# Performance work log

Measured on AMD Instinct MI355X. Metric: run time of the kernel, lower is better.

The kernel has to match this reference:

```python
import jax, jax.numpy as jnp
import numpy as np

HIDDEN = 768
HEADS = 12
HEAD_DIM = HIDDEN // HEADS


def setup_inputs() -> dict:
    key = jax.random.key(0)
    ks = jax.random.split(key, 6)
    B, N = 32, 577  # N = 1 CLS + 576 patches
    x = jax.random.normal(ks[0], (B, N, HIDDEN), dtype=jnp.float32)
    seg_bias = jax.random.uniform(ks[1], (B, N - 1), dtype=jnp.float32)
    w_qkv = jax.random.normal(ks[2], (HIDDEN, 3 * HIDDEN), dtype=jnp.float32) * 0.02
    b_qkv = jnp.zeros((3 * HIDDEN,), dtype=jnp.float32)
    w_proj = jax.random.normal(ks[3], (HIDDEN, HIDDEN), dtype=jnp.float32) * 0.02
    b_proj = jnp.zeros((HIDDEN,), dtype=jnp.float32)
    seg_scale = jnp.ones((), dtype=jnp.float32)
    return {"x": x, "seg_bias": seg_bias, "w_qkv": w_qkv, "b_qkv": b_qkv,
            "w_proj": w_proj, "b_proj": b_proj, "seg_scale": seg_scale}


def reference(x, seg_bias, w_qkv, b_qkv, w_proj, b_proj, seg_scale):
    B, N, _ = x.shape
    scale = HEAD_DIM ** -0.5
    qkv = x @ w_qkv + b_qkv                       # (B, N, 3*H*D)
    qkv = qkv.reshape(B, N, 3, HEADS, HEAD_DIM)
    q = qkv[:, :, 0].transpose(0, 2, 1, 3)        # (B, H, N, D)
    k = qkv[:, :, 1].transpose(0, 2, 1, 3)
    v = qkv[:, :, 2].transpose(0, 2, 1, 3)
    attn = jnp.einsum('bhqd,bhkd->bhqk', q, k) * scale  # (B, H, N, N)
    # additive seg bias on CLS-query row, patch keys only (cols 1:)
    bias = (seg_bias * seg_scale)[:, None, None, :]     # (B,1,1,N-1)
    attn = attn.at[:, :, 0:1, 1:].add(bias)
    attn = jax.nn.softmax(attn, axis=-1)
    out = jnp.einsum('bhqk,bhkd->bhqd', attn, v)        # (B, H, N, D)
    out = out.transpose(0, 2, 1, 3).reshape(B, N, HIDDEN)
    return out @ w_proj + b_proj
```

## Files before the change

### kernel.cpp

```cpp
#include <hip/hip_runtime.h>


typedef unsigned short bf16_t;
typedef __attribute__((ext_vector_type(8))) short short8;
typedef __attribute__((ext_vector_type(4))) float f32x4;

#define B_    32
#define N_    577
#define BN_   18464
#define HID_  768
#define NH_   12
#define HD_   64
#define QKVC_ 2304
#define NPAD_ 640

__device__ __forceinline__ bf16_t f2bf(float f) {
  union { float f; unsigned u; } x; x.f = f;
  unsigned r = x.u + 0x7fffu + ((x.u >> 16) & 1u);
  return (bf16_t)(r >> 16);
}

__global__ __launch_bounds__(256) void cast_kernel(const float* __restrict__ in,
                                                   bf16_t* __restrict__ out, int n4) {
  int i = blockIdx.x * 256 + threadIdx.x;
  if (i >= n4) return;
  float4 v = ((const float4*)in)[i];
  ushort4 o;
  o.x = f2bf(v.x); o.y = f2bf(v.y); o.z = f2bf(v.z); o.w = f2bf(v.w);
  ((ushort4*)out)[i] = o;
}

__global__ __launch_bounds__(256) void transpose_cast_kernel(const float* __restrict__ in,
                                                             bf16_t* __restrict__ out,
                                                             int R, int C) {
  __shared__ float tile[32][33];
  int c0 = blockIdx.x * 32, r0 = blockIdx.y * 32;
  int tx = threadIdx.x, ty = threadIdx.y;
  #pragma unroll
  for (int i = ty; i < 32; i += 8)
    tile[i][tx] = in[(size_t)(r0 + i) * C + c0 + tx];
  __syncthreads();
  #pragma unroll
  for (int i = ty; i < 32; i += 8)
    out[(size_t)(c0 + i) * R + r0 + tx] = f2bf(tile[tx][i]);
}

template <int OUT_BF16>
__global__ __launch_bounds__(256, 3) void gemm_bf16_kernel(
    const bf16_t* __restrict__ A,
    const bf16_t* __restrict__ Bt,
    const float* __restrict__ bias,
    void* __restrict__ Cout,
    int M, int Nc) {
  __shared__ bf16_t As[128 * 64];
  __shared__ bf16_t Bs[128 * 64];

  const int tid  = threadIdx.x;
  const int lane = tid & 63, w = tid >> 6;
  const int quad = lane >> 4, l16 = lane & 15;

  const int Mb = (M + 127) >> 7;
  const int Nb = Nc >> 7;
  const int np_full = Mb >> 3;
  const int rem = Mb - np_full * 8;
  int bid = blockIdx.x;
  int m_blk, n_blk;
  int body = np_full * 8 * Nb;
  if (bid < body) {
    int p = bid / (8 * Nb), local = bid % (8 * Nb);
    m_blk = p * 8 + (local & 7);
    n_blk = local >> 3;
  } else {
    int t = bid - body;
    m_blk = np_full * 8 + t % rem;
    n_blk = t / rem;
  }
  const int m0 = m_blk * 128, n0 = n_blk * 128;
  const int wm = (w >> 1) * 64, wn = (w & 1) * 64;

  f32x4 acc[4][4];
  #pragma unroll
  for (int i = 0; i < 4; ++i)
    #pragma unroll
    for (int j = 0; j < 4; ++j)
      acc[i][j] = (f32x4){0.f, 0.f, 0.f, 0.f};

  for (int kt = 0; kt < 768; kt += 64) {
    __syncthreads();
    #pragma unroll
    for (int it = 0; it < 4; ++it) {
      int gi = it * 256 + tid;
      int row = gi >> 3, chp = gi & 7;
      int ch = chp ^ (row & 7);
      int gm = m0 + row; if (gm >= M) gm = M - 1;
      __builtin_amdgcn_global_load_lds(
          (const __attribute__((address_space(1))) unsigned int*)(A + (size_t)gm * 768 + kt + ch * 8),
          (__attribute__((address_space(3))) unsigned int*)(As + gi * 8),
          16, 0, 0);
      int gn = n0 + row;
      __builtin_amdgcn_global_load_lds(
          (const __attribute__((address_space(1))) unsigned int*)(Bt + (size_t)gn * 768 + kt + ch * 8),
          (__attribute__((address_space(3))) unsigned int*)(Bs + gi * 8),
          16, 0, 0);
    }
    __syncthreads();

    #pragma unroll
    for (int ks = 0; ks < 2; ++ks) {
      short8 af[4], bfr[4];
      #pragma unroll
      for (int i = 0; i < 4; ++i) {
        int row = wm + i * 16 + l16;
        int c = ks * 4 + quad;
        af[i] = *(const short8*)(As + row * 64 + (c ^ (row & 7)) * 8);
      }
      #pragma unroll
      for (int j = 0; j < 4; ++j) {
        int row = wn + j * 16 + l16;
        int c = ks * 4 + quad;
        bfr[j] = *(const short8*)(Bs + row * 64 + (c ^ (row & 7)) * 8);
      }
      #pragma unroll
      for (int i = 0; i < 4; ++i)
        #pragma unroll
        for (int j = 0; j < 4; ++j)
          acc[i][j] = __builtin_amdgcn_mfma_f32_16x16x32_bf16(af[i], bfr[j], acc[i][j], 0, 0, 0);
    }
  }

  #pragma unroll
  for (int i = 0; i < 4; ++i) {
    int mrow_base = m0 + wm + i * 16 + quad * 4;
    #pragma unroll
    for (int j = 0; j < 4; ++j) {
      int col = n0 + wn + j * 16 + l16;
      float bs = bias[col];
      #pragma unroll
      for (int r = 0; r < 4; ++r) {
        int row = mrow_base + r;
        if (row < M) {
          float v = acc[i][j][r] + bs;
          if (OUT_BF16)
            ((bf16_t*)Cout)[(size_t)row * Nc + col] = f2bf(v);
          else
            ((float*)Cout)[(size_t)row * Nc + col] = v;
        }
      }
    }
  }
}

__global__ __launch_bounds__(256) void vt_kernel(const bf16_t* __restrict__ qkv,
                                                 bf16_t* __restrict__ vT) {
  const int t = blockIdx.x, h = blockIdx.y, b = blockIdx.z;
  const int tid = threadIdx.x;
  __shared__ bf16_t Ls[64 * 65];
  const int kv0 = t * 64;
  const bf16_t* Vp = qkv + (size_t)b * N_ * QKVC_ + 2 * HID_ + h * HD_;

  #pragma unroll
  for (int it = 0; it < 2; ++it) {
    int idx = it * 256 + tid;
    int row = idx >> 3, ch = idx & 7;
    int krow = kv0 + row; if (krow > N_ - 1) krow = N_ - 1;
    short8 v8 = *(const short8*)(Vp + (size_t)krow * QKVC_ + ch * 8);
    #pragma unroll
    for (int j = 0; j < 8; ++j)
      Ls[(ch * 8 + j) * 65 + row] = (bf16_t)v8[j];
  }
  __syncthreads();
  bf16_t* outp = vT + ((size_t)(b * NH_ + h) * HD_) * NPAD_;
  #pragma unroll
  for (int it = 0; it < 2; ++it) {
    int idx = it * 256 + tid;
    int d = idx >> 3, kc = idx & 7;
    short8 o8;
    #pragma unroll
    for (int j = 0; j < 8; ++j)
      o8[j] = (short)Ls[d * 65 + kc * 8 + j];
    *(short8*)(outp + (size_t)d * NPAD_ + kv0 + kc * 8) = o8;
  }
}

__global__ __launch_bounds__(256) void attn_kernel(
    const bf16_t* __restrict__ qkv,
    const bf16_t* __restrict__ vT,
    const float* __restrict__ seg_bias,
    const float* __restrict__ seg_scale,
    bf16_t* __restrict__ out) {
  const int bid  = blockIdx.x;
  const int pair = bid % (B_ * NH_);
  const int qt   = bid / (B_ * NH_);
  const int h    = pair % NH_;
  const int b    = pair / NH_;
  const int tid = threadIdx.x;
  const int w = tid >> 6, lane = tid & 63;
  const int quad = lane >> 4, l16 = lane & 15;

  __shared__ bf16_t Ks[2][64 * 72];
  __shared__ bf16_t Vt[2][64 * 72];
  __shared__ bf16_t Pb[4][32 * 72];

  const bf16_t* Qbase = qkv + (size_t)b * N_ * QKVC_ + h * HD_;
  const bf16_t* Kbase = Qbase + HID_;
  const bf16_t* Vtb   = vT + ((size_t)(b * NH_ + h) * HD_) * NPAD_;

  const int q0 = qt * 128 + w * 32;
  short8 qf[2][2];
  #pragma unroll
  for (int mi = 0; mi < 2; ++mi) {
    int qr = q0 + mi * 16 + l16;
    if (qr > N_ - 1) qr = N_ - 1;
    qf[mi][0] = *(const short8*)(Qbase + (size_t)qr * QKVC_ + quad * 8);
    qf[mi][1] = *(const short8*)(Qbase + (size_t)qr * QKVC_ + 32 + quad * 8);
  }
  const float qsc = 0.125f * 1.44269504f;
  #pragma unroll
  for (int mi = 0; mi < 2; ++mi)
    #pragma unroll
    for (int c = 0; c < 2; ++c)
      #pragma unroll
      for (int j = 0; j < 8; ++j) {
        unsigned u = ((unsigned)(unsigned short)qf[mi][c][j]) << 16;
        union { unsigned u; float f; } x; x.u = u;
        qf[mi][c][j] = (short)f2bf(x.f * qsc);
      }

  f32x4 o[2][4];
  float lsum[2][4];
  #pragma unroll
  for (int mi = 0; mi < 2; ++mi)
    #pragma unroll
    for (int j = 0; j < 4; ++j) {
      o[mi][j] = (f32x4){0.f, 0.f, 0.f, 0.f};
      lsum[mi][j] = 0.f;
    }

  const float ssl = seg_scale[0] * 1.44269504f;
  const bool bias_wave = (qt == 0 && w == 0);
  bf16_t* pw = Pb[w];

  const int srow = tid >> 3;
  const int sch  = tid & 7;

  short8 kpre[2], vpre[2];
  #pragma unroll
  for (int it = 0; it < 2; ++it) {
    int row = it * 32 + srow;
    int krow = row; if (krow > N_ - 1) krow = N_ - 1;
    kpre[it] = *(const short8*)(Kbase + (size_t)krow * QKVC_ + sch * 8);
    vpre[it] = *(const short8*)(Vtb + (size_t)row * NPAD_ + sch * 8);
  }
  #pragma unroll
  for (int it = 0; it < 2; ++it) {
    int row = it * 32 + srow;
    *(short8*)(&Ks[0][0] + row * 72 + sch * 8) = kpre[it];
    *(short8*)(&Vt[0][0] + row * 72 + sch * 8) = vpre[it];
  }
  __syncthreads();

  for (int t = 0; t < 10; ++t) {
    const int cur = t & 1;
    const int kv0 = t * 64;
    const bf16_t* ks = &Ks[cur][0];
    const bf16_t* vt = &Vt[cur][0];

    if (t < 9) {
      const int kv1 = kv0 + 64;
      #pragma unroll
      for (int it = 0; it < 2; ++it) {
        int row = it * 32 + srow;
        int krow = kv1 + row; if (krow > N_ - 1) krow = N_ - 1;
        kpre[it] = *(const short8*)(Kbase + (size_t)krow * QKVC_ + sch * 8);
        vpre[it] = *(const short8*)(Vtb + (size_t)row * NPAD_ + kv1 + sch * 8);
      }
    }

    f32x4 s[2][4];
    #pragma unroll
    for (int mi = 0; mi < 2; ++mi)
      #pragma unroll
      for (int sub = 0; sub < 4; ++sub)
        s[mi][sub] = (f32x4){0.f, 0.f, 0.f, 0.f};
    #pragma unroll
    for (int sub = 0; sub < 4; ++sub) {
      short8 k0 = *(const short8*)(ks + (sub * 16 + l16) * 72 + quad * 8);
      short8 k1 = *(const short8*)(ks + (sub * 16 + l16) * 72 + 32 + quad * 8);
      #pragma unroll
      for (int mi = 0; mi < 2; ++mi) {
        s[mi][sub] = __builtin_amdgcn_mfma_f32_16x16x32_bf16(qf[mi][0], k0, s[mi][sub], 0, 0, 0);
        s[mi][sub] = __builtin_amdgcn_mfma_f32_16x16x32_bf16(qf[mi][1], k1, s[mi][sub], 0, 0, 0);
      }
    }

    if (bias_wave && quad == 0) {
      #pragma unroll
      for (int sub = 0; sub < 4; ++sub) {
        int key = kv0 + sub * 16 + l16;
        if (key >= 1 && key < N_)
          s[0][sub][0] += seg_bias[b * (N_ - 1) + key - 1] * ssl;
      }
    }

    #pragma unroll
    for (int mi = 0; mi < 2; ++mi)
      #pragma unroll
      for (int sub = 0; sub < 4; ++sub) {
        #pragma unroll
        for (int r = 0; r < 4; ++r) {
          float p = exp2f(s[mi][sub][r]);
          if (t == 9) {
            int key = kv0 + sub * 16 + l16;
            if (key >= N_) p = 0.f;
          }
          lsum[mi][r] += p;
          union { float f; unsigned u; } c; c.f = p;
          pw[(mi * 16 + r * 4 + quad) * 72 + sub * 16 + l16] =
              (bf16_t)((c.u + 0x8000u) >> 16);
        }
      }

    #pragma unroll
    for (int mi = 0; mi < 2; ++mi) {
      int prow = mi * 16 + ((l16 & 3) << 2) + (l16 >> 2);
      short8 pa0 = *(const short8*)(pw + prow * 72 + quad * 8);
      short8 pa1 = *(const short8*)(pw + prow * 72 + 32 + quad * 8);
      #pragma unroll
      for (int ds = 0; ds < 4; ++ds) {
        short8 vb0 = *(const short8*)(vt + (ds * 16 + l16) * 72 + quad * 8);
        short8 vb1 = *(const short8*)(vt + (ds * 16 + l16) * 72 + 32 + quad * 8);
        o[mi][ds] = __builtin_amdgcn_mfma_f32_16x16x32_bf16(pa0, vb0, o[mi][ds], 0, 0, 0);
        o[mi][ds] = __builtin_amdgcn_mfma_f32_16x16x32_bf16(pa1, vb1, o[mi][ds], 0, 0, 0);
      }
    }

    if (t < 9) {
      bf16_t* ksn = &Ks[1 - cur][0];
      bf16_t* vtn = &Vt[1 - cur][0];
      #pragma unroll
      for (int it = 0; it < 2; ++it) {
        int row = it * 32 + srow;
        *(short8*)(ksn + row * 72 + sch * 8) = kpre[it];
        *(short8*)(vtn + row * 72 + sch * 8) = vpre[it];
      }
    }
    __syncthreads();
  }

  #pragma unroll
  for (int mi = 0; mi < 2; ++mi)
    #pragma unroll
    for (int r = 0; r < 4; ++r) {
      float l = lsum[mi][r];
      #pragma unroll
      for (int off = 1; off < 16; off <<= 1)
        l += __shfl_xor(l, off);
      float inv = 1.0f / l;
      int row = q0 + mi * 16 + quad * 4 + r;
      if (row < N_) {
        size_t base = ((size_t)b * N_ + row) * HID_ + h * HD_;
        #pragma unroll
        for (int ds = 0; ds < 4; ++ds)
          out[base + ds * 16 + l16] = f2bf(o[mi][ds][r] * inv);
      }
    }
}

extern "C" void kernel_launch(void* const* d_in, const int* in_sizes, int n_in,
                              void* d_out, int out_size, void* d_ws, size_t ws_size,
                              hipStream_t stream) {
  const float* x         = (const float*)d_in[0];
  const float* seg_bias  = (const float*)d_in[1];
  const float* w_qkv     = (const float*)d_in[2];
  const float* b_qkv     = (const float*)d_in[3];
  const float* w_proj    = (const float*)d_in[4];
  const float* b_proj    = (const float*)d_in[5];
  const float* seg_scale = (const float*)d_in[6];

  char* ws = (char*)d_ws;
  bf16_t* xb     = (bf16_t*)ws;
  bf16_t* wqkvT  = (bf16_t*)(ws + 28360704);
  bf16_t* wprojT = (bf16_t*)(ws + 31899648);
  bf16_t* qkvb   = (bf16_t*)(ws + 33079296);
  bf16_t* vT     = (bf16_t*)(ws + 118161408);
  bf16_t* attnb  = xb;

  cast_kernel<<<(BN_ * HID_ / 4) / 256, 256, 0, stream>>>(x, xb, BN_ * HID_ / 4);
  dim3 tb(32, 8);
  transpose_cast_kernel<<<dim3(QKVC_ / 32, HID_ / 32), tb, 0, stream>>>(w_qkv, wqkvT, HID_, QKVC_);
  transpose_cast_kernel<<<dim3(HID_ / 32, HID_ / 32), tb, 0, stream>>>(w_proj, wprojT, HID_, HID_);

  gemm_bf16_kernel<1><<<145 * (QKVC_ / 128), 256, 0, stream>>>(
      xb, wqkvT, b_qkv, (void*)qkvb, BN_, QKVC_);

  vt_kernel<<<dim3(10, NH_, B_), 256, 0, stream>>>(qkvb, vT);

  attn_kernel<<<5 * NH_ * B_, 256, 0, stream>>>(qkvb, vT, seg_bias, seg_scale, attnb);

  gemm_bf16_kernel<0><<<145 * (HID_ / 128), 256, 0, stream>>>(
      attnb, wprojT, b_proj, d_out, BN_, HID_);
}
```

Baseline: 342.1 us.

## Keep softmax probabilities in registers via transposed QK^T MFMA layout

```diff
diff --git a/kernel.cpp b/kernel.cpp
--- a/kernel.cpp
+++ b/kernel.cpp
@@ -3,6 +3,7 @@
 
 typedef unsigned short bf16_t;
 typedef __attribute__((ext_vector_type(8))) short short8;
+typedef __attribute__((ext_vector_type(4))) short short4v;
 typedef __attribute__((ext_vector_type(4))) float f32x4;
 
 #define B_    32
@@ -18,6 +19,16 @@
   union { float f; unsigned u; } x; x.f = f;
   unsigned r = x.u + 0x7fffu + ((x.u >> 16) & 1u);
   return (bf16_t)(r >> 16);
+}
+
+__device__ __forceinline__ short4v pack4_bf16(f32x4 p) {
+  short4v o;
+  #pragma unroll
+  for (int j = 0; j < 4; ++j) {
+    union { float f; unsigned u; } c; c.f = p[j];
+    o[j] = (short)((c.u + 0x8000u) >> 16);
+  }
+  return o;
 }
 
 __global__ __launch_bounds__(256) void cast_kernel(const float* __restrict__ in,
@@ -182,7 +193,7 @@
   }
 }
 
-__global__ __launch_bounds__(256) void attn_kernel(
+__global__ __launch_bounds__(256, 4) void attn_kernel(
     const bf16_t* __restrict__ qkv,
     const bf16_t* __restrict__ vT,
     const float* __restrict__ seg_bias,
@@ -199,7 +210,6 @@
 
   __shared__ bf16_t Ks[2][64 * 72];
   __shared__ bf16_t Vt[2][64 * 72];
-  __shared__ bf16_t Pb[4][32 * 72];
 
   const bf16_t* Qbase = qkv + (size_t)b * N_ * QKVC_ + h * HD_;
   const bf16_t* Kbase = Qbase + HID_;
@@ -227,18 +237,15 @@
       }
 
   f32x4 o[2][4];
-  float lsum[2][4];
+  float lsum[2] = {0.f, 0.f};
   #pragma unroll
   for (int mi = 0; mi < 2; ++mi)
     #pragma unroll
-    for (int j = 0; j < 4; ++j) {
+    for (int j = 0; j < 4; ++j)
       o[mi][j] = (f32x4){0.f, 0.f, 0.f, 0.f};
-      lsum[mi][j] = 0.f;
-    }
 
   const float ssl = seg_scale[0] * 1.44269504f;
-  const bool bias_wave = (qt == 0 && w == 0);
-  bf16_t* pw = Pb[w];
+  const bool bias_lane = (qt == 0 && w == 0 && l16 == 0);
 
   const int srow = tid >> 3;
   const int sch  = tid & 7;
@@ -288,49 +295,49 @@
       short8 k1 = *(const short8*)(ks + (sub * 16 + l16) * 72 + 32 + quad * 8);
       #pragma unroll
       for (int mi = 0; mi < 2; ++mi) {
-        s[mi][sub] = __builtin_amdgcn_mfma_f32_16x16x32_bf16(qf[mi][0], k0, s[mi][sub], 0, 0, 0);
-        s[mi][sub] = __builtin_amdgcn_mfma_f32_16x16x32_bf16(qf[mi][1], k1, s[mi][sub], 0, 0, 0);
-      }
-    }
-
-    if (bias_wave && quad == 0) {
+        s[mi][sub] = __builtin_amdgcn_mfma_f32_16x16x32_bf16(k0, qf[mi][0], s[mi][sub], 0, 0, 0);
+        s[mi][sub] = __builtin_amdgcn_mfma_f32_16x16x32_bf16(k1, qf[mi][1], s[mi][sub], 0, 0, 0);
+      }
+    }
+
+    if (bias_lane) {
+      #pragma unroll
+      for (int sub = 0; sub < 4; ++sub)
+        #pragma unroll
+        for (int r = 0; r < 4; ++r) {
+          int key = kv0 + sub * 16 + quad * 4 + r;
+          if (key >= 1 && key < N_)
+            s[0][sub][r] += seg_bias[b * (N_ - 1) + key - 1] * ssl;
+        }
+    }
+
+    short4v pf[2][4];
+    #pragma unroll
+    for (int mi = 0; mi < 2; ++mi)
       #pragma unroll
       for (int sub = 0; sub < 4; ++sub) {
-        int key = kv0 + sub * 16 + l16;
-        if (key >= 1 && key < N_)
-          s[0][sub][0] += seg_bias[b * (N_ - 1) + key - 1] * ssl;
-      }
-    }
-
-    #pragma unroll
-    for (int mi = 0; mi < 2; ++mi)
-      #pragma unroll
-      for (int sub = 0; sub < 4; ++sub) {
+        f32x4 p4;
         #pragma unroll
         for (int r = 0; r < 4; ++r) {
           float p = exp2f(s[mi][sub][r]);
           if (t == 9) {
-            int key = kv0 + sub * 16 + l16;
+            int key = kv0 + sub * 16 + quad * 4 + r;
             if (key >= N_) p = 0.f;
           }
-          lsum[mi][r] += p;
-          union { float f; unsigned u; } c; c.f = p;
-          pw[(mi * 16 + r * 4 + quad) * 72 + sub * 16 + l16] =
-              (bf16_t)((c.u + 0x8000u) >> 16);
+          lsum[mi] += p;
+          p4[r] = p;
         }
-      }
-
-    #pragma unroll
-    for (int mi = 0; mi < 2; ++mi) {
-      int prow = mi * 16 + ((l16 & 3) << 2) + (l16 >> 2);
-      short8 pa0 = *(const short8*)(pw + prow * 72 + quad * 8);
-      short8 pa1 = *(const short8*)(pw + prow * 72 + 32 + quad * 8);
-      #pragma unroll
-      for (int ds = 0; ds < 4; ++ds) {
-        short8 vb0 = *(const short8*)(vt + (ds * 16 + l16) * 72 + quad * 8);
-        short8 vb1 = *(const short8*)(vt + (ds * 16 + l16) * 72 + 32 + quad * 8);
-        o[mi][ds] = __builtin_amdgcn_mfma_f32_16x16x32_bf16(pa0, vb0, o[mi][ds], 0, 0, 0);
-        o[mi][ds] = __builtin_amdgcn_mfma_f32_16x16x32_bf16(pa1, vb1, o[mi][ds], 0, 0, 0);
+        pf[mi][sub] = pack4_bf16(p4);
+      }
+
+    #pragma unroll
+    for (int ds = 0; ds < 4; ++ds) {
+      #pragma unroll
+      for (int sub = 0; sub < 4; ++sub) {
+        short4v vb = *(const short4v*)(vt + (ds * 16 + l16) * 72 + sub * 16 + quad * 4);
+        #pragma unroll
+        for (int mi = 0; mi < 2; ++mi)
+          o[mi][ds] = __builtin_amdgcn_mfma_f32_16x16x16bf16_1k(pf[mi][sub], vb, o[mi][ds], 0, 0, 0);
       }
     }
 
@@ -348,15 +355,16 @@
   }
 
   #pragma unroll
-  for (int mi = 0; mi < 2; ++mi)
+  for (int mi = 0; mi < 2; ++mi) {
+    float l = lsum[mi];
+    l += __shfl_xor(l, 16);
+    l += __shfl_xor(l, 32);
     #pragma unroll
     for (int r = 0; r < 4; ++r) {
-      float l = lsum[mi][r];
-      #pragma unroll
-      for (int off = 1; off < 16; off <<= 1)
-        l += __shfl_xor(l, off);
-      float inv = 1.0f / l;
-      int row = q0 + mi * 16 + quad * 4 + r;
+      int rowl = quad * 4 + r;
+      float lr = __shfl(l, (lane & 48) + rowl);
+      float inv = 1.0f / lr;
+      int row = q0 + mi * 16 + rowl;
       if (row < N_) {
         size_t base = ((size_t)b * N_ + row) * HID_ + h * HD_;
         #pragma unroll
@@ -364,6 +372,7 @@
           out[base + ds * 16 + l16] = f2bf(o[mi][ds][r] * inv);
       }
     }
+  }
 }
 
 extern "C" void kernel_launch(void* const* d_in, const int* in_sizes, int n_in,
```

Result: slower. 373.6 us (+9.2%).
